# Optimization experiments

Hardware: AMD Instinct MI355X
Metric: run time of the kernel (lower is better)

## Reference

```python
import jax, jax.numpy as jnp
import numpy as np

N_HEADS = 16
HEAD_DIM = 64
D_MODEL = N_HEADS * HEAD_DIM  # 1024


def setup_inputs() -> dict:
    key = jax.random.key(0)
    ks = jax.random.split(key, 6)
    B, S, D = 2, 2048, D_MODEL
    s = 0.02
    return {
        "hidden_states": jax.random.normal(ks[0], (B, S, D), jnp.float32),
        "position_bias": jax.random.normal(ks[1], (1, N_HEADS, S, S), jnp.float32),
        "Wq": jax.random.normal(ks[2], (D, D), jnp.float32) * s,
        "Wk": jax.random.normal(ks[3], (D, D), jnp.float32) * s,
        "Wv": jax.random.normal(ks[4], (D, D), jnp.float32) * s,
        "Wo": jax.random.normal(ks[5], (D, D), jnp.float32) * s,
    }


def reference(hidden_states, position_bias, Wq, Wk, Wv, Wo):
    B, S, D = hidden_states.shape

    def split_heads(x):  # [B,S,D] -> [B,H,S,hd]
        return x.reshape(B, S, N_HEADS, HEAD_DIM).transpose(0, 2, 1, 3)

    q = split_heads(hidden_states @ Wq)
    k = split_heads(hidden_states @ Wk)
    v = split_heads(hidden_states @ Wv)

    # T5 attention: NO 1/sqrt(d) scaling; additive relative-position bias.
    scores = jnp.einsum("bhqd,bhkd->bhqk", q, k) + position_bias
    attn = jax.nn.softmax(scores.astype(jnp.float32), axis=-1).astype(scores.dtype)
    ctx = jnp.einsum("bhqk,bhkd->bhqd", attn, v)
    ctx = ctx.transpose(0, 2, 1, 3).reshape(B, S, D)
    return ctx @ Wo
```

## Files before the change

kernel.cpp:

```cpp
#include <hip/hip_runtime.h>
#include <hip/hip_bf16.h>
#include <stdint.h>

typedef __bf16 bf16_t;
typedef __bf16 bf16x4 __attribute__((ext_vector_type(4)));
typedef __bf16 bf16x8 __attribute__((ext_vector_type(8)));
typedef float  f32x4  __attribute__((ext_vector_type(4)));

#define S_LEN 2048
#define NH    16
#define HD    64
#define DM    1024
#define BATCH 2
#define M_TOT (BATCH * S_LEN)
#define SM_SHIFT 18.0f

__device__ __forceinline__ void gload16(const void* g, void* l) {
    __builtin_amdgcn_global_load_lds(
        (const __attribute__((address_space(1))) unsigned int*)g,
        (__attribute__((address_space(3))) unsigned int*)l, 16, 0, 0);
}

__global__ void convert_h(const float* __restrict__ X, bf16_t* __restrict__ Y, int n) {
    int i = (blockIdx.x * 256 + threadIdx.x) * 4;
    if (i >= n) return;
    float4 v = *(const float4*)(X + i);
    union { bf16_t h[4]; uint2 u; } pk;
    pk.h[0] = (bf16_t)v.x; pk.h[1] = (bf16_t)v.y;
    pk.h[2] = (bf16_t)v.z; pk.h[3] = (bf16_t)v.w;
    *(uint2*)(Y + i) = pk.u;
}

__global__ void convert_transpose_w4(const float* __restrict__ W0, const float* __restrict__ W1,
                                     const float* __restrict__ W2, const float* __restrict__ W3,
                                     bf16_t* __restrict__ D0, bf16_t* __restrict__ D3) {
    __shared__ float tile[32][33];
    const int z = blockIdx.z;
    const float* W = z == 0 ? W0 : z == 1 ? W1 : z == 2 ? W2 : W3;
    bf16_t* Wt = z < 3 ? D0 + (size_t)z * DM * DM : D3;
    const int tid = threadIdx.x;
    const int tx = tid & 31, ty = tid >> 5;
    const int bx = blockIdx.x * 32, by = blockIdx.y * 32;
#pragma unroll
    for (int it = 0; it < 4; ++it)
        tile[ty + it * 8][tx] = W[(size_t)(by + ty + it * 8) * DM + bx + tx];
    __syncthreads();
#pragma unroll
    for (int it = 0; it < 4; ++it)
        Wt[(size_t)(bx + ty + it * 8) * DM + by + tx] = (bf16_t)tile[tx][ty + it * 8];
}

template<int BN, int EPI>
__global__ __launch_bounds__(256)
void gemm_glds(const bf16_t* __restrict__ A, const bf16_t* __restrict__ Bt,
               float* __restrict__ Cf, bf16_t* __restrict__ Qb, bf16_t* __restrict__ Kb,
               bf16_t* __restrict__ Vtb, int M, int N, int K)
{
    constexpr int WN = BN / 2;
    constexpr int NJ = WN / 16;
    constexpr int RB = BN / 32;
    __shared__ bf16_t smem[16640];
    bf16_t* At  = smem;
    bf16_t* Bts = smem + 8192;

    const int tid  = threadIdx.x;
    const int lane = tid & 63;
    const int wave = tid >> 6;
    const int lc = lane & 15;
    const int l4 = lane >> 4;
    const int wr = wave >> 1, wc = wave & 1;
    const int m0 = blockIdx.y * 128;
    const int n0 = blockIdx.x * BN;
    const int srow = tid >> 3;
    const int scol = (tid & 7) * 8;

    f32x4 acc[4][NJ] = {};

    for (int k0 = 0; k0 < K; k0 += 64) {
        __syncthreads();
#pragma unroll
        for (int ro = 0; ro < 4; ++ro)
            gload16(A + (size_t)(m0 + ro * 32 + srow) * K + k0 + scol,
                    At + ro * 2048 + wave * 512);
#pragma unroll
        for (int ro = 0; ro < RB; ++ro)
            gload16(Bt + (size_t)(n0 + ro * 32 + srow) * K + k0 + scol,
                    Bts + ro * 2048 + wave * 512);
        __syncthreads();

        bf16x8 af[2][4], bfr[2][NJ];
#pragma unroll
        for (int kk = 0; kk < 2; ++kk) {
#pragma unroll
            for (int i = 0; i < 4; ++i)
                af[kk][i] = *(const bf16x8*)(At + (wr * 64 + i * 16 + lc) * 64 + kk * 32 + l4 * 8);
#pragma unroll
            for (int j = 0; j < NJ; ++j)
                bfr[kk][j] = *(const bf16x8*)(Bts + (wc * WN + j * 16 + lc) * 64 + kk * 32 + l4 * 8);
        }
#pragma unroll
        for (int kk = 0; kk < 2; ++kk)
#pragma unroll
            for (int i = 0; i < 4; ++i)
#pragma unroll
                for (int j = 0; j < NJ; ++j)
                    acc[i][j] = __builtin_amdgcn_mfma_f32_16x16x32_bf16(af[kk][i], bfr[kk][j], acc[i][j], 0, 0, 0);
    }

    if (EPI == 1) {
#pragma unroll
        for (int i = 0; i < 4; ++i)
#pragma unroll
            for (int j = 0; j < NJ; ++j)
#pragma unroll
                for (int r = 0; r < 4; ++r) {
                    int m = m0 + wr * 64 + i * 16 + l4 * 4 + r;
                    int n = n0 + wc * WN + j * 16 + lc;
                    Cf[(size_t)m * N + n] = acc[i][j][r];
                }
    } else {
        const int sel = n0 >> 10;
        if (sel < 2) {
            bf16_t* Dst = sel == 0 ? Qb : Kb;
#pragma unroll
            for (int i = 0; i < 4; ++i)
#pragma unroll
                for (int j = 0; j < NJ; ++j)
#pragma unroll
                    for (int r = 0; r < 4; ++r) {
                        int m = m0 + wr * 64 + i * 16 + l4 * 4 + r;
                        int n = (n0 & 1023) + wc * WN + j * 16 + lc;
                        int b = m >> 11, s = m & 2047, h = n >> 6, d = n & 63;
                        Dst[(((size_t)(b * NH + h)) * S_LEN + s) * HD + d] = (bf16_t)acc[i][j][r];
                    }
        } else {
            __syncthreads();
            bf16_t* Ct = smem;
#pragma unroll
            for (int i = 0; i < 4; ++i)
#pragma unroll
                for (int j = 0; j < NJ; ++j)
#pragma unroll
                    for (int r = 0; r < 4; ++r) {
                        int ml = wr * 64 + i * 16 + l4 * 4 + r;
                        int nl = wc * WN + j * 16 + lc;
                        Ct[nl * 130 + ml] = (bf16_t)acc[i][j][r];
                    }
            __syncthreads();
            const int rr = tid >> 1, c0 = (tid & 1) * 64;
            const int nn = (n0 - 2048) + rr;
            const int hh = nn >> 6, dd = nn & 63;
            const int bb = m0 >> 11, s0 = m0 & 2047;
            bf16_t* dst = Vtb + (((size_t)(bb * NH + hh)) * HD + dd) * S_LEN + s0 + c0;
            const bf16_t* srcr = Ct + rr * 130 + c0;
#pragma unroll
            for (int u = 0; u < 8; ++u)
                *(uint4*)(dst + u * 8) = *(const uint4*)(srcr + u * 8);
        }
    }
}

__global__ __launch_bounds__(512, 1)
void attn_kernel(const bf16_t* __restrict__ Q, const bf16_t* __restrict__ Kin,
                 const bf16_t* __restrict__ Vt, const float* __restrict__ bias,
                 bf16_t* __restrict__ Ctx)
{
    const int tid  = threadIdx.x;
    const int lane = tid & 63;
    const int wave = tid >> 6;
    const int b    = wave >> 2;
    const int ws   = wave & 3;
    const int lc = lane & 15;
    const int l4 = lane >> 4;

    const int f   = blockIdx.x;
    const int xcd = f & 7;
    const int kk_ = f >> 3;
    const int h   = xcd * 2 + (kk_ >> 4);
    const int qt  = kk_ & 15;
    const int qw  = qt * 128 + ws * 32;

    __shared__ bf16_t Kt[2][2][64 * 64];
    __shared__ bf16_t Vs[2][2][64 * 64];
    __shared__ float  Bs[2][128 * 64];

    const bf16_t* Qg = Q + (size_t)(b * NH + h) * S_LEN * HD;
    const bf16_t* Kg[2]; const bf16_t* Vg[2];
#pragma unroll
    for (int bb = 0; bb < 2; ++bb) {
        Kg[bb] = Kin + (size_t)(bb * NH + h) * S_LEN * HD;
        Vg[bb] = Vt  + (size_t)(bb * NH + h) * HD * S_LEN;
    }
    const float* Bg = bias + (size_t)h * S_LEN * S_LEN;

    bf16x8 qf[2][2];
#pragma unroll
    for (int i = 0; i < 2; ++i)
#pragma unroll
        for (int kk = 0; kk < 2; ++kk)
            qf[i][kk] = *(const bf16x8*)(Qg + (size_t)(qw + i * 16 + lc) * HD + kk * 32 + l4 * 8);

    f32x4 cacc[2][4] = {};
    float lsum[2] = {};

    const int r0   = lane >> 3;
    const int gsrc = (lane & 7) ^ r0;
    const int R    = wave * 8;

    auto stageKV = [&](int t, int pbuf) {
        const int kv0 = t * 64;
        gload16(Kg[0] + (size_t)(kv0 + R + r0) * HD + gsrc * 8, &Kt[0][pbuf][R * 64]);
        gload16(Kg[1] + (size_t)(kv0 + R + r0) * HD + gsrc * 8, &Kt[1][pbuf][R * 64]);
        gload16(Vg[0] + (size_t)(R + r0) * S_LEN + kv0 + gsrc * 8, &Vs[0][pbuf][R * 64]);
        gload16(Vg[1] + (size_t)(R + r0) * S_LEN + kv0 + gsrc * 8, &Vs[1][pbuf][R * 64]);
    };

    const int br4 = lane >> 4;
    const int bcg = lane & 15;
    auto stageB = [&](int t, int pbuf) {
        const int kv0 = t * 64;
#pragma unroll
        for (int c = 0; c < 4; ++c) {
            const int ql = wave * 16 + c * 4 + br4;
            const int sg = bcg ^ ((c & 1) * 4 + br4);
            gload16(Bg + (size_t)(qt * 128 + ql) * S_LEN + kv0 + sg * 4,
                    (char*)&Bs[pbuf][0] + (wave * 4 + c) * 1024);
        }
    };

    stageKV(0, 0);
    stageB(0, 0);

    for (int t = 0; t < 32; ++t) {
        const int buf = t & 1;
        __builtin_amdgcn_sched_barrier(0);
        asm volatile("s_waitcnt lgkmcnt(0)" ::: "memory");
        asm volatile("s_waitcnt vmcnt(0)" ::: "memory");
        __builtin_amdgcn_s_barrier();
        __builtin_amdgcn_sched_barrier(0);
        if (t < 31) {
            stageKV(t + 1, buf ^ 1);
            stageB(t + 1, buf ^ 1);
        }
        __builtin_amdgcn_sched_barrier(0);

        f32x4 bv[2][4];
        const float* Bbuf = &Bs[buf][0];
#pragma unroll
        for (int i = 0; i < 2; ++i)
#pragma unroll
            for (int j = 0; j < 4; ++j) {
                const int ql = ws * 32 + i * 16 + lc;
                bv[i][j] = *(const f32x4*)(Bbuf + ql * 64 + (((4 * j + l4) ^ (lc & 7)) * 4));
            }

        f32x4 saT[4][2] = {};
        __builtin_amdgcn_s_setprio(1);
#pragma unroll
        for (int kk = 0; kk < 2; ++kk) {
            bf16x8 kf[4];
#pragma unroll
            for (int j = 0; j < 4; ++j)
                kf[j] = *(const bf16x8*)(&Kt[b][buf][(j * 16 + lc) * 64 + (((kk * 4 + l4) ^ (lc & 7)) * 8)]);
#pragma unroll
            for (int j = 0; j < 4; ++j)
#pragma unroll
                for (int i = 0; i < 2; ++i)
                    saT[j][i] = __builtin_amdgcn_mfma_f32_16x16x32_bf16(kf[j], qf[i][kk], saT[j][i], 0, 0, 0);
        }
        __builtin_amdgcn_s_setprio(0);

        union { uint32_t d[4]; bf16x8 v; } pa[2][2];
#pragma unroll
        for (int i = 0; i < 2; ++i) {
            f32x4 pe[4];
#pragma unroll
            for (int j = 0; j < 4; ++j) {
                f32x4 s = (saT[j][i] - SM_SHIFT) + bv[i][j];
                pe[j].x = __expf(s.x); pe[j].y = __expf(s.y);
                pe[j].z = __expf(s.z); pe[j].w = __expf(s.w);
                lsum[i] += (pe[j].x + pe[j].y) + (pe[j].z + pe[j].w);
            }
#pragma unroll
            for (int ks = 0; ks < 2; ++ks) {
                asm("v_cvt_pk_bf16_f32 %0, %1, %2" : "=v"(pa[i][ks].d[0]) : "v"(pe[2*ks].x),   "v"(pe[2*ks].y));
                asm("v_cvt_pk_bf16_f32 %0, %1, %2" : "=v"(pa[i][ks].d[1]) : "v"(pe[2*ks].z),   "v"(pe[2*ks].w));
                asm("v_cvt_pk_bf16_f32 %0, %1, %2" : "=v"(pa[i][ks].d[2]) : "v"(pe[2*ks+1].x), "v"(pe[2*ks+1].y));
                asm("v_cvt_pk_bf16_f32 %0, %1, %2" : "=v"(pa[i][ks].d[3]) : "v"(pe[2*ks+1].z), "v"(pe[2*ks+1].w));
            }
        }

        __builtin_amdgcn_s_setprio(1);
#pragma unroll
        for (int ks = 0; ks < 2; ++ks) {
#pragma unroll
            for (int jd = 0; jd < 4; ++jd) {
                union { bf16x4 h[2]; bf16x8 v; } vv;
                const int row = jd * 16 + lc;
                vv.h[0] = *(const bf16x4*)(&Vs[b][buf][row * 64 + (((4 * ks +     (l4 >> 1)) ^ (lc & 7)) * 8) + 4 * (l4 & 1)]);
                vv.h[1] = *(const bf16x4*)(&Vs[b][buf][row * 64 + (((4 * ks + 2 + (l4 >> 1)) ^ (lc & 7)) * 8) + 4 * (l4 & 1)]);
#pragma unroll
                for (int i = 0; i < 2; ++i)
                    cacc[i][jd] = __builtin_amdgcn_mfma_f32_16x16x32_bf16(pa[i][ks].v, vv.v, cacc[i][jd], 0, 0, 0);
            }
        }
        __builtin_amdgcn_s_setprio(0);
    }

#pragma unroll
    for (int i = 0; i < 2; ++i) {
        lsum[i] += __shfl_xor(lsum[i], 16, 64);
        lsum[i] += __shfl_xor(lsum[i], 32, 64);
    }
    float rinv[2][4];
#pragma unroll
    for (int i = 0; i < 2; ++i)
#pragma unroll
        for (int r = 0; r < 4; ++r)
            rinv[i][r] = 1.0f / __shfl(lsum[i], l4 * 4 + r, 16);

    bf16_t* Co = Ctx + (size_t)b * S_LEN * DM + (size_t)h * HD;
#pragma unroll
    for (int i = 0; i < 2; ++i)
#pragma unroll
        for (int r = 0; r < 4; ++r) {
            int qrow = qw + i * 16 + l4 * 4 + r;
#pragma unroll
            for (int jd = 0; jd < 4; ++jd)
                Co[(size_t)qrow * DM + jd * 16 + lc] = (bf16_t)(cacc[i][jd][r] * rinv[i][r]);
        }
}

extern "C" void kernel_launch(void* const* d_in, const int* in_sizes, int n_in,
                              void* d_out, int out_size, void* d_ws, size_t ws_size,
                              hipStream_t stream)
{
    (void)in_sizes; (void)n_in; (void)out_size; (void)ws_size;
    const float* hs   = (const float*)d_in[0];
    const float* bias = (const float*)d_in[1];
    const float* Wq   = (const float*)d_in[2];
    const float* Wk   = (const float*)d_in[3];
    const float* Wv   = (const float*)d_in[4];
    const float* Wo   = (const float*)d_in[5];
    float* out = (float*)d_out;

    char* ws = (char*)d_ws;
    bf16_t* Hbf   = (bf16_t*)(ws);
    bf16_t* Wqkvt = (bf16_t*)(ws + ( 8u << 20));
    bf16_t* Wot   = (bf16_t*)(ws + (14u << 20));
    bf16_t* Qb    = (bf16_t*)(ws + (16u << 20));
    bf16_t* Kb    = (bf16_t*)(ws + (24u << 20));
    bf16_t* Vtb   = (bf16_t*)(ws + (32u << 20));
    bf16_t* Ctx   = (bf16_t*)(ws + (40u << 20));

    convert_h<<<4096, 256, 0, stream>>>(hs, Hbf, M_TOT * DM);
    dim3 tg(32, 32, 4);
    convert_transpose_w4<<<tg, 256, 0, stream>>>(Wq, Wk, Wv, Wo, Wqkvt, Wot);

    dim3 gq(3 * DM / 128, M_TOT / 128);
    gemm_glds<128, 0><<<gq, 256, 0, stream>>>(Hbf, Wqkvt, nullptr, Qb, Kb, Vtb,
                                              M_TOT, 3 * DM, DM);

    attn_kernel<<<256, 512, 0, stream>>>(Qb, Kb, Vtb, bias, Ctx);

    dim3 go(DM / 64, M_TOT / 128);
    gemm_glds<64, 1><<<go, 256, 0, stream>>>(Ctx, Wot, out, nullptr, nullptr, nullptr,
                                             M_TOT, DM, DM);
}
```

Measured before the change: 182.0 us.

## Split attention into smaller blocks with 64-query tiles and 32-key steps

The attention kernel now launches 512 blocks of 256 threads, each handling 64 queries for both batches, instead of 256 blocks of 512 threads handling 128 queries. The KV step shrinks from 64 to 32 keys, with loop count, LDS tile shapes, swizzles and staging loads adjusted to match. The aim is more blocks across the CUs and less LDS per block, at the cost of twice as many barrier-synchronised iterations with less MFMA work between each barrier.

Result: slower. 187.9 us (+3.2%).

```diff
diff --git a/kernel.cpp b/kernel.cpp
--- a/kernel.cpp
+++ b/kernel.cpp
@@ -160,7 +160,7 @@
     }
 }
 
-__global__ __launch_bounds__(512, 1)
+__global__ __launch_bounds__(256, 1)
 void attn_kernel(const bf16_t* __restrict__ Q, const bf16_t* __restrict__ Kin,
                  const bf16_t* __restrict__ Vt, const float* __restrict__ bias,
                  bf16_t* __restrict__ Ctx)
@@ -168,21 +168,21 @@
     const int tid  = threadIdx.x;
     const int lane = tid & 63;
     const int wave = tid >> 6;
-    const int b    = wave >> 2;
-    const int ws   = wave & 3;
+    const int b    = wave >> 1;
+    const int ws   = wave & 1;
     const int lc = lane & 15;
     const int l4 = lane >> 4;
 
     const int f   = blockIdx.x;
     const int xcd = f & 7;
-    const int kk_ = f >> 3;
-    const int h   = xcd * 2 + (kk_ >> 4);
-    const int qt  = kk_ & 15;
-    const int qw  = qt * 128 + ws * 32;
-
-    __shared__ bf16_t Kt[2][2][64 * 64];
-    __shared__ bf16_t Vs[2][2][64 * 64];
-    __shared__ float  Bs[2][128 * 64];
+    const int idx = f >> 3;
+    const int h   = xcd * 2 + (idx >> 5);
+    const int qt  = idx & 31;
+    const int qw  = qt * 64 + ws * 32;
+
+    __shared__ bf16_t Kt[2][2][32 * 64];
+    __shared__ bf16_t Vs[2][2][64 * 32];
+    __shared__ float  Bs[2][64 * 32];
 
     const bf16_t* Qg = Q + (size_t)(b * NH + h) * S_LEN * HD;
     const bf16_t* Kg[2]; const bf16_t* Vg[2];
@@ -203,106 +203,99 @@
     f32x4 cacc[2][4] = {};
     float lsum[2] = {};
 
-    const int r0   = lane >> 3;
-    const int gsrc = (lane & 7) ^ r0;
-    const int R    = wave * 8;
+    const int r0 = lane >> 3;
+    const int gK = (lane & 7) ^ r0;
+    const int rv = lane >> 2;
+    const int gV = (lane & 3) ^ ((rv >> 1) & 3);
+    const int gB = (lane & 7) ^ r0;
+    const int R8 = wave * 8;
+    const int Rv = wave * 16;
 
     auto stageKV = [&](int t, int pbuf) {
-        const int kv0 = t * 64;
-        gload16(Kg[0] + (size_t)(kv0 + R + r0) * HD + gsrc * 8, &Kt[0][pbuf][R * 64]);
-        gload16(Kg[1] + (size_t)(kv0 + R + r0) * HD + gsrc * 8, &Kt[1][pbuf][R * 64]);
-        gload16(Vg[0] + (size_t)(R + r0) * S_LEN + kv0 + gsrc * 8, &Vs[0][pbuf][R * 64]);
-        gload16(Vg[1] + (size_t)(R + r0) * S_LEN + kv0 + gsrc * 8, &Vs[1][pbuf][R * 64]);
+        const int kv0 = t * 32;
+        gload16(Kg[0] + (size_t)(kv0 + R8 + r0) * HD + gK * 8, &Kt[0][pbuf][R8 * 64]);
+        gload16(Kg[1] + (size_t)(kv0 + R8 + r0) * HD + gK * 8, &Kt[1][pbuf][R8 * 64]);
+        gload16(Vg[0] + (size_t)(Rv + rv) * S_LEN + kv0 + gV * 8, &Vs[0][pbuf][Rv * 32]);
+        gload16(Vg[1] + (size_t)(Rv + rv) * S_LEN + kv0 + gV * 8, &Vs[1][pbuf][Rv * 32]);
     };
-
-    const int br4 = lane >> 4;
-    const int bcg = lane & 15;
     auto stageB = [&](int t, int pbuf) {
-        const int kv0 = t * 64;
-#pragma unroll
-        for (int c = 0; c < 4; ++c) {
-            const int ql = wave * 16 + c * 4 + br4;
-            const int sg = bcg ^ ((c & 1) * 4 + br4);
-            gload16(Bg + (size_t)(qt * 128 + ql) * S_LEN + kv0 + sg * 4,
-                    (char*)&Bs[pbuf][0] + (wave * 4 + c) * 1024);
+        const int kv0 = t * 32;
+#pragma unroll
+        for (int c = 0; c < 2; ++c) {
+            const int Rb = wave * 16 + c * 8;
+            gload16(Bg + (size_t)(qt * 64 + Rb + r0) * S_LEN + kv0 + gB * 4,
+                    &Bs[pbuf][Rb * 32]);
         }
     };
 
     stageKV(0, 0);
     stageB(0, 0);
 
-    for (int t = 0; t < 32; ++t) {
+    for (int t = 0; t < 64; ++t) {
         const int buf = t & 1;
         __builtin_amdgcn_sched_barrier(0);
         asm volatile("s_waitcnt lgkmcnt(0)" ::: "memory");
         asm volatile("s_waitcnt vmcnt(0)" ::: "memory");
         __builtin_amdgcn_s_barrier();
         __builtin_amdgcn_sched_barrier(0);
-        if (t < 31) {
+        if (t < 63) {
             stageKV(t + 1, buf ^ 1);
             stageB(t + 1, buf ^ 1);
         }
         __builtin_amdgcn_sched_barrier(0);
 
-        f32x4 bv[2][4];
-        const float* Bbuf = &Bs[buf][0];
-#pragma unroll
-        for (int i = 0; i < 2; ++i)
-#pragma unroll
-            for (int j = 0; j < 4; ++j) {
-                const int ql = ws * 32 + i * 16 + lc;
-                bv[i][j] = *(const f32x4*)(Bbuf + ql * 64 + (((4 * j + l4) ^ (lc & 7)) * 4));
-            }
-
-        f32x4 saT[4][2] = {};
+        f32x4 bv[2][2];
+#pragma unroll
+        for (int i = 0; i < 2; ++i) {
+            const int q = ws * 32 + i * 16 + lc;
+#pragma unroll
+            for (int j = 0; j < 2; ++j)
+                bv[i][j] = *(const f32x4*)(&Bs[buf][q * 32 + (((j * 4 + l4) ^ (lc & 7)) * 4)]);
+        }
+
+        f32x4 saT[2][2] = {};
         __builtin_amdgcn_s_setprio(1);
 #pragma unroll
         for (int kk = 0; kk < 2; ++kk) {
-            bf16x8 kf[4];
-#pragma unroll
-            for (int j = 0; j < 4; ++j)
+            bf16x8 kf[2];
+#pragma unroll
+            for (int j = 0; j < 2; ++j)
                 kf[j] = *(const bf16x8*)(&Kt[b][buf][(j * 16 + lc) * 64 + (((kk * 4 + l4) ^ (lc & 7)) * 8)]);
 #pragma unroll
-            for (int j = 0; j < 4; ++j)
+            for (int j = 0; j < 2; ++j)
 #pragma unroll
                 for (int i = 0; i < 2; ++i)
                     saT[j][i] = __builtin_amdgcn_mfma_f32_16x16x32_bf16(kf[j], qf[i][kk], saT[j][i], 0, 0, 0);
         }
         __builtin_amdgcn_s_setprio(0);
 
-        union { uint32_t d[4]; bf16x8 v; } pa[2][2];
+        union { uint32_t d[4]; bf16x8 v; } pa[2];
 #pragma unroll
         for (int i = 0; i < 2; ++i) {
-            f32x4 pe[4];
-#pragma unroll
-            for (int j = 0; j < 4; ++j) {
+            f32x4 pe[2];
+#pragma unroll
+            for (int j = 0; j < 2; ++j) {
                 f32x4 s = (saT[j][i] - SM_SHIFT) + bv[i][j];
                 pe[j].x = __expf(s.x); pe[j].y = __expf(s.y);
                 pe[j].z = __expf(s.z); pe[j].w = __expf(s.w);
                 lsum[i] += (pe[j].x + pe[j].y) + (pe[j].z + pe[j].w);
             }
-#pragma unroll
-            for (int ks = 0; ks < 2; ++ks) {
-                asm("v_cvt_pk_bf16_f32 %0, %1, %2" : "=v"(pa[i][ks].d[0]) : "v"(pe[2*ks].x),   "v"(pe[2*ks].y));
-                asm("v_cvt_pk_bf16_f32 %0, %1, %2" : "=v"(pa[i][ks].d[1]) : "v"(pe[2*ks].z),   "v"(pe[2*ks].w));
-                asm("v_cvt_pk_bf16_f32 %0, %1, %2" : "=v"(pa[i][ks].d[2]) : "v"(pe[2*ks+1].x), "v"(pe[2*ks+1].y));
-                asm("v_cvt_pk_bf16_f32 %0, %1, %2" : "=v"(pa[i][ks].d[3]) : "v"(pe[2*ks+1].z), "v"(pe[2*ks+1].w));
-            }
+            asm("v_cvt_pk_bf16_f32 %0, %1, %2" : "=v"(pa[i].d[0]) : "v"(pe[0].x), "v"(pe[0].y));
+            asm("v_cvt_pk_bf16_f32 %0, %1, %2" : "=v"(pa[i].d[1]) : "v"(pe[0].z), "v"(pe[0].w));
+            asm("v_cvt_pk_bf16_f32 %0, %1, %2" : "=v"(pa[i].d[2]) : "v"(pe[1].x), "v"(pe[1].y));
+            asm("v_cvt_pk_bf16_f32 %0, %1, %2" : "=v"(pa[i].d[3]) : "v"(pe[1].z), "v"(pe[1].w));
         }
 
         __builtin_amdgcn_s_setprio(1);
 #pragma unroll
-        for (int ks = 0; ks < 2; ++ks) {
-#pragma unroll
-            for (int jd = 0; jd < 4; ++jd) {
-                union { bf16x4 h[2]; bf16x8 v; } vv;
-                const int row = jd * 16 + lc;
-                vv.h[0] = *(const bf16x4*)(&Vs[b][buf][row * 64 + (((4 * ks +     (l4 >> 1)) ^ (lc & 7)) * 8) + 4 * (l4 & 1)]);
-                vv.h[1] = *(const bf16x4*)(&Vs[b][buf][row * 64 + (((4 * ks + 2 + (l4 >> 1)) ^ (lc & 7)) * 8) + 4 * (l4 & 1)]);
-#pragma unroll
-                for (int i = 0; i < 2; ++i)
-                    cacc[i][jd] = __builtin_amdgcn_mfma_f32_16x16x32_bf16(pa[i][ks].v, vv.v, cacc[i][jd], 0, 0, 0);
-            }
+        for (int jd = 0; jd < 4; ++jd) {
+            union { bf16x4 hh[2]; bf16x8 v; } vv;
+            const int row = jd * 16 + lc;
+            vv.hh[0] = *(const bf16x4*)(&Vs[b][buf][row * 32 + ((((l4 >> 1))     ^ ((row >> 1) & 3)) * 8) + (l4 & 1) * 4]);
+            vv.hh[1] = *(const bf16x4*)(&Vs[b][buf][row * 32 + (((2 + (l4 >> 1)) ^ ((row >> 1) & 3)) * 8) + (l4 & 1) * 4]);
+#pragma unroll
+            for (int i = 0; i < 2; ++i)
+                cacc[i][jd] = __builtin_amdgcn_mfma_f32_16x16x32_bf16(pa[i].v, vv.v, cacc[i][jd], 0, 0, 0);
         }
         __builtin_amdgcn_s_setprio(0);
     }
@@ -361,7 +354,7 @@
     gemm_glds<128, 0><<<gq, 256, 0, stream>>>(Hbf, Wqkvt, nullptr, Qb, Kb, Vtb,
                                               M_TOT, 3 * DM, DM);
 
-    attn_kernel<<<256, 512, 0, stream>>>(Qb, Kb, Vtb, bias, Ctx);
+    attn_kernel<<<512, 256, 0, stream>>>(Qb, Kb, Vtb, bias, Ctx);
 
     dim3 go(DM / 64, M_TOT / 128);
     gemm_glds<64, 1><<<go, 256, 0, stream>>>(Ctx, Wot, out, nullptr, nullptr, nullptr,
```
